# Kernel tuning notes

Measured on AMD Instinct MI355X. Metric: run time of the kernel, lower is better.

## Reference

```python
import jax, jax.numpy as jnp
import numpy as np

H = 32        # num query heads
HKV = 8       # num kv heads
D = 128       # head_dim
SCALE = D ** -0.5
FP8_MAX = 448.0   # e4m3 max
EPS = 1e-8
PAGE = 256
NPAGES = 20
SQ = 1024     # new diffusion tokens
CTX = 3072    # cached context tokens
DIFF_BLK = 32 # diffusion block size


def setup_inputs() -> dict:
    key = jax.random.key(0)
    ks = jax.random.split(key, 6)
    q = jax.random.normal(ks[0], (SQ, H * D), dtype=jnp.float32)
    k = jax.random.normal(ks[1], (SQ, HKV * D), dtype=jnp.float32)
    v = jax.random.normal(ks[2], (SQ, HKV * D), dtype=jnp.float32)
    # paged caches (values already stored in quantized units)
    k_cache = jax.random.normal(ks[3], (NPAGES, PAGE, HKV, D), dtype=jnp.float32)
    v_cache = jax.random.normal(ks[4], (NPAGES, PAGE, HKV, D), dtype=jnp.float32)
    # new tokens go into slots right after the context
    slot_mapping = jnp.arange(CTX, CTX + SQ, dtype=jnp.int32)
    cache_slots = jnp.arange(CTX, dtype=jnp.int32)
    # diffusion mask: full visibility of context, block-causal among new tokens
    blk = jnp.arange(SQ) // DIFF_BLK
    ctx_mask = jnp.ones((SQ, CTX), dtype=bool)
    new_mask = blk[:, None] >= blk[None, :]
    block_mask = jnp.concatenate([ctx_mask, new_mask], axis=1)  # [SQ, CTX+SQ]
    return {"q": q, "k": k, "v": v, "k_cache": k_cache, "v_cache": v_cache,
            "slot_mapping": slot_mapping, "cache_slots": cache_slots,
            "block_mask": block_mask}


def reference(q, k, v, k_cache, v_cache, slot_mapping, cache_slots, block_mask):
    k3 = k.reshape(-1, HKV, D)
    v3 = v.reshape(-1, HKV, D)
    qh = q.reshape(-1, H, D)

    # ---- FP8 scale tracking: per-kv-head absmax over (token, dim) ----
    k_scale = jnp.maximum(jnp.max(jnp.abs(k3), axis=(0, 2)) / FP8_MAX, EPS)  # [HKV]
    v_scale = jnp.maximum(jnp.max(jnp.abs(v3), axis=(0, 2)) / FP8_MAX, EPS)

    # ---- paged KV-cache store with inline quantization ----
    kc = k_cache.reshape(-1, HKV, D)  # [NPAGES*PAGE, HKV, D]
    vc = v_cache.reshape(-1, HKV, D)
    k_q = jnp.clip(k3 / k_scale[None, :, None], -FP8_MAX, FP8_MAX)
    v_q = jnp.clip(v3 / v_scale[None, :, None], -FP8_MAX, FP8_MAX)
    kc = kc.at[slot_mapping].set(k_q)
    vc = vc.at[slot_mapping].set(v_q)

    # ---- load context tokens from cache and dequantize ----
    k_ctx = kc[cache_slots] * k_scale[None, :, None]  # [CTX, HKV, D]
    v_ctx = vc[cache_slots] * v_scale[None, :, None]
    k_comb = jnp.concatenate([k_ctx, k3], axis=0)  # [SKV, HKV, D]
    v_comb = jnp.concatenate([v_ctx, v3], axis=0)

    # ---- GQA flex attention with token-level block mask ----
    G = H // HKV
    k_g = jnp.repeat(k_comb, G, axis=1)  # [SKV, H, D]
    v_g = jnp.repeat(v_comb, G, axis=1)
    scores = jnp.einsum('qhd,khd->hqk', qh, k_g) * SCALE  # [H, SQ, SKV]
    scores = jnp.where(block_mask[None, :, :], scores, jnp.float32(-1e30))
    probs = jax.nn.softmax(scores, axis=-1)
    o = jnp.einsum('hqk,khd->qhd', probs, v_g)  # [SQ, H, D]
    return o.reshape(-1, H * D)
```

## Files before the change

kernel.cpp:

```cpp
#include <hip/hip_runtime.h>
#include <stdint.h>

#define H 32
#define HKV 8
#define D 128
#define SQ 1024
#define CTX 3072
#define SKV 4096
#define FP8_MAX_C 448.0f
#define EPS_C 1e-8f

typedef __attribute__((ext_vector_type(4))) float f32x4;
typedef __attribute__((ext_vector_type(8))) __bf16 bf16x8;
typedef __attribute__((ext_vector_type(8))) unsigned short u16x8;

__device__ __forceinline__ unsigned short f2bf(float x) {
  unsigned int u = __builtin_bit_cast(unsigned int, x);
  u += 0x7fffu + ((u >> 16) & 1u);
  return (unsigned short)(u >> 16);
}

__device__ __forceinline__ f32x4 mfma16(bf16x8 a, bf16x8 b, f32x4 c) {
  return __builtin_amdgcn_mfma_f32_16x16x32_bf16(a, b, c, 0, 0, 0);
}

__device__ __forceinline__ void gld16(const unsigned short* g, char* l) {
  __builtin_amdgcn_global_load_lds(
      (const __attribute__((address_space(1))) unsigned int*)g,
      (__attribute__((address_space(3))) unsigned int*)l, 16, 0, 0);
}

__device__ __forceinline__ void stage_sync() {
  asm volatile("s_waitcnt vmcnt(0)" ::: "memory");
  __builtin_amdgcn_sched_barrier(0);
  __syncthreads();
}

__global__ void scales_part(const float* __restrict__ k,
                            const float* __restrict__ v,
                            unsigned int* __restrict__ smax) {
  const int b = blockIdx.x & 15;
  const int part = blockIdx.x >> 4;
  const float* src = (b < HKV) ? k : v;
  const int h = b & 7;
  const int tid = threadIdx.x;
  const int d0 = (tid & 31) * 4;
  float mx = 0.f;
  const int t1 = part * 128 + 128;
  for (int t = part * 128 + (tid >> 5); t < t1; t += 8) {
    float4 vv = *reinterpret_cast<const float4*>(src + (size_t)t * (HKV * D) + h * D + d0);
    mx = fmaxf(mx, fmaxf(fmaxf(fabsf(vv.x), fabsf(vv.y)),
                         fmaxf(fabsf(vv.z), fabsf(vv.w))));
  }
  __shared__ float red[256];
  red[tid] = mx;
  __syncthreads();
  for (int s = 128; s > 0; s >>= 1) {
    if (tid < s) red[tid] = fmaxf(red[tid], red[tid + s]);
    __syncthreads();
  }
  if (tid == 0) atomicMax(&smax[b], __float_as_uint(red[0]));
}

__global__ void scales_fin(const unsigned int* __restrict__ smax,
                           float* __restrict__ scales) {
  const int i = threadIdx.x;
  if (i < 16) scales[i] = fmaxf(__uint_as_float(smax[i]) / FP8_MAX_C, EPS_C);
}

__global__ void prep_k(const float* __restrict__ k,
                       const float* __restrict__ k_cache,
                       const int* __restrict__ cache_slots,
                       const float* __restrict__ scales,
                       unsigned short* __restrict__ k_comb) {
  const int tid = blockIdx.x * 256 + threadIdx.x;
  const int d8 = tid & 15;
  const int t = (tid >> 4) & (SKV - 1);
  const int h = tid >> 16;
  const int d0 = d8 * 8;
  const float* src;
  float mul;
  if (t < CTX) {
    int slot = cache_slots[t];
    src = k_cache + (size_t)slot * (HKV * D) + h * D + d0;
    mul = scales[h];
  } else {
    src = k + (size_t)(t - CTX) * (HKV * D) + h * D + d0;
    mul = 1.f;
  }
  float4 a = *reinterpret_cast<const float4*>(src);
  float4 bb = *reinterpret_cast<const float4*>(src + 4);
  u16x8 r;
  r[0] = f2bf(a.x * mul);  r[1] = f2bf(a.y * mul);
  r[2] = f2bf(a.z * mul);  r[3] = f2bf(a.w * mul);
  r[4] = f2bf(bb.x * mul); r[5] = f2bf(bb.y * mul);
  r[6] = f2bf(bb.z * mul); r[7] = f2bf(bb.w * mul);
  *reinterpret_cast<u16x8*>(k_comb + ((size_t)h * SKV + t) * D + d0) = r;
}

__global__ void prep_v(const float* __restrict__ v,
                       const float* __restrict__ v_cache,
                       const int* __restrict__ cache_slots,
                       const float* __restrict__ scales,
                       unsigned short* __restrict__ v_combT) {
  const int tid = blockIdx.x * 256 + threadIdx.x;
  const int d = tid & 127;
  const int t8 = (tid >> 7) & 511;
  const int h = tid >> 16;
  const int t0 = t8 * 8;
  const float sc = scales[8 + h];
  u16x8 r;
#pragma unroll
  for (int i = 0; i < 8; ++i) {
    int t = t0 + i;
    float val;
    if (t < CTX) {
      int slot = cache_slots[t];
      val = v_cache[(size_t)slot * (HKV * D) + h * D + d] * sc;
    } else {
      val = v[(size_t)(t - CTX) * (HKV * D) + h * D + d];
    }
    r[i] = f2bf(val);
  }
  *reinterpret_cast<u16x8*>(v_combT + ((size_t)h * D + d) * SKV + t0) = r;
}

#define LDBF(p) (*reinterpret_cast<const bf16x8*>(p))
#define Z4 ((f32x4){0.f, 0.f, 0.f, 0.f})

#define STAGE(TB, BUFO)                                                        \
  {                                                                            \
    _Pragma("unroll")                                                          \
    for (int j = 0; j < 4; ++j) {                                              \
      const int c = wid * 256 + j * 64 + l;                                    \
      const int r_ = c >> 4;                                                   \
      const int lc_ = (c & 15) ^ (r_ & 7);                                     \
      gld16(kb + (size_t)((TB) + r_) * D + lc_ * 8,                            \
            smem + (BUFO) + c * 16);                                           \
      const int dv_ = c >> 3;                                                  \
      const int lv_ = (c & 7) ^ (dv_ & 7);                                     \
      gld16(vb + (size_t)dv_ * SKV + (TB) + lv_ * 8,                           \
            smem + (BUFO) + 16384 + c * 16);                                   \
    }                                                                          \
  }

#define EXP4(SREG, P, RSV)                                                     \
  {                                                                            \
    P[0] = __builtin_amdgcn_exp2f(SREG[0] - m);                                \
    P[1] = __builtin_amdgcn_exp2f(SREG[1] - m);                                \
    P[2] = __builtin_amdgcn_exp2f(SREG[2] - m);                                \
    P[3] = __builtin_amdgcn_exp2f(SREG[3] - m);                                \
    RSV += (P[0] + P[1]) + (P[2] + P[3]);                                      \
  }

#define CVTPK(DST, LO, HI)                                                     \
  asm("v_cvt_pk_bf16_f32 %0, %1, %2" : "=v"(DST) : "v"(LO), "v"(HI));
#define SW32(A, B)                                                             \
  asm("v_permlane32_swap_b32 %0, %1" : "+v"(A), "+v"(B));
#define SW16(A, B)                                                             \
  asm("v_permlane16_swap_b32 %0, %1" : "+v"(A), "+v"(B));

#define PTRANS(P0, P1, P2, P3, PF0, PF1)                                       \
  {                                                                            \
    unsigned int A_, Ap_, B_, Bp_, C_, Cp_, Dd_, Dp_;                          \
    CVTPK(A_, P0[0], P0[1]) CVTPK(Ap_, P0[2], P0[3])                           \
    CVTPK(B_, P1[0], P1[1]) CVTPK(Bp_, P1[2], P1[3])                           \
    CVTPK(C_, P2[0], P2[1]) CVTPK(Cp_, P2[2], P2[3])                           \
    CVTPK(Dd_, P3[0], P3[1]) CVTPK(Dp_, P3[2], P3[3])                          \
    SW32(A_, B_) SW16(A_, B_)                                                  \
    SW32(Ap_, Bp_) SW16(Ap_, Bp_)                                              \
    SW32(C_, Dd_) SW16(C_, Dd_)                                                \
    SW32(Cp_, Dp_) SW16(Cp_, Dp_)                                              \
    union { unsigned int d[4]; bf16x8 v; } u0_, u1_;                           \
    u0_.d[0] = A_; u0_.d[1] = Ap_; u0_.d[2] = B_; u0_.d[3] = Bp_;              \
    u1_.d[0] = C_; u1_.d[1] = Cp_; u1_.d[2] = Dd_; u1_.d[3] = Dp_;             \
    PF0 = u0_.v; PF1 = u1_.v;                                                  \
  }

#define QKSF(SF, SA, SB)                                                       \
  {                                                                            \
    bf16x8 a0 = LDBF(kc + SF * 4096 + kx0);                                    \
    bf16x8 a1 = LDBF(kc + SF * 4096 + kx1);                                    \
    bf16x8 a2 = LDBF(kc + SF * 4096 + kx2);                                    \
    bf16x8 a3 = LDBF(kc + SF * 4096 + kx3);                                    \
    SA = mfma16(a0, qa0, SA); SA = mfma16(a1, qa1, SA);                        \
    SA = mfma16(a2, qa2, SA); SA = mfma16(a3, qa3, SA);                        \
    SB = mfma16(a0, qb0, SB); SB = mfma16(a1, qb1, SB);                        \
    SB = mfma16(a2, qb2, SB); SB = mfma16(a3, qb3, SB);                        \
  }

#define PVDT(DT, AA, AB)                                                       \
  {                                                                            \
    bf16x8 va = LDBF(vc + DT * 2048 + vxa);                                    \
    bf16x8 vw = LDBF(vc + DT * 2048 + vxb);                                    \
    AA = mfma16(pfa0, va, AA); AA = mfma16(pfa1, vw, AA);                      \
    AB = mfma16(pfb0, va, AB); AB = mfma16(pfb1, vw, AB);                      \
  }

__launch_bounds__(256, 2)
__global__ void attn_kernel(const float* __restrict__ q,
                            const unsigned short* __restrict__ k_comb,
                            const unsigned short* __restrict__ v_combT,
                            float* __restrict__ out,
                            float* __restrict__ part1,
                            float* __restrict__ ml) {
  extern __shared__ __align__(16) char smem[];
  const int bid = blockIdx.x;
  const int hkv = bid & 7;
  const int qp_raw = (bid >> 3) & 31;
  const int half = bid >> 8;
  const int qp = half ? (31 - qp_raw) : qp_raw;
  const int tid = threadIdx.x;
  const int wid = tid >> 6;
  const int l = tid & 63;
  const int lo = l & 15;
  const int g = l >> 4;
  const int qbase = qp * 32 + (wid >> 1) * 16;
  const int hqa = hkv * 4 + (wid & 1) * 2;
  const int nt32 = 97 + qp;
  const int n64 = (nt32 + 1) >> 1;
  const int nh = (n64 + 1) >> 1;
  const int t0 = half ? nh : 0;
  const int t1 = half ? n64 : nh;
  const bool tail = (nt32 & 1) && half;

  const unsigned short* kb = k_comb + (size_t)hkv * SKV * D;
  const unsigned short* vb = v_combT + (size_t)hkv * D * SKV;

  bf16x8 qa0, qa1, qa2, qa3, qb0, qb1, qb2, qb3;
  {
    const float qs = 0.088388347648318447f * 1.4426950408889634f;
    const float* qpA = q + (size_t)(qbase + lo) * (H * D) + hqa * D;
#define QLOAD(PTR, KS, DST)                                                    \
    {                                                                          \
      float4 a = *reinterpret_cast<const float4*>((PTR) + KS * 32 + g * 8);    \
      float4 b = *reinterpret_cast<const float4*>((PTR) + KS * 32 + g * 8 + 4);\
      union { unsigned short u[8]; bf16x8 v; } f;                              \
      f.u[0] = f2bf(a.x * qs); f.u[1] = f2bf(a.y * qs);                        \
      f.u[2] = f2bf(a.z * qs); f.u[3] = f2bf(a.w * qs);                        \
      f.u[4] = f2bf(b.x * qs); f.u[5] = f2bf(b.y * qs);                        \
      f.u[6] = f2bf(b.z * qs); f.u[7] = f2bf(b.w * qs);                        \
      DST = f.v;                                                               \
    }
    QLOAD(qpA, 0, qa0) QLOAD(qpA, 1, qa1) QLOAD(qpA, 2, qa2) QLOAD(qpA, 3, qa3)
    const float* qpB = qpA + D;
    QLOAD(qpB, 0, qb0) QLOAD(qpB, 1, qb1) QLOAD(qpB, 2, qb2) QLOAD(qpB, 3, qb3)
#undef QLOAD
  }

  f32x4 aa0 = Z4, aa1 = Z4, aa2 = Z4, aa3 = Z4;
  f32x4 aa4 = Z4, aa5 = Z4, aa6 = Z4, aa7 = Z4;
  f32x4 ab0 = Z4, ab1 = Z4, ab2 = Z4, ab3 = Z4;
  f32x4 ab4 = Z4, ab5 = Z4, ab6 = Z4, ab7 = Z4;
  float m = -1e30f;
  float lsa = 0.f, lsb = 0.f;

  const int xr = lo & 7;
  const int kx0 = ((0 + g) ^ xr) << 4;
  const int kx1 = ((4 + g) ^ xr) << 4;
  const int kx2 = ((8 + g) ^ xr) << 4;
  const int kx3 = ((12 + g) ^ xr) << 4;
  const int vxa = ((g) ^ xr) << 4;
  const int vxb = ((g + 4) ^ xr) << 4;
  const char* kbl = smem + lo * 256;
  const char* vbl = smem + 16384 + lo * 128;

  int cur = 0;
  STAGE(t0 * 64, 0)
  stage_sync();

  for (int t = t0; t < t1; ++t) {
    if (t + 1 < t1) STAGE((t + 1) * 64, (cur ^ 1) * 32768)

    const char* kc = kbl + cur * 32768;
    const char* vc = vbl + cur * 32768;

    f32x4 sa0 = Z4, sa1 = Z4, sa2 = Z4, sa3 = Z4;
    f32x4 sb0 = Z4, sb1 = Z4, sb2 = Z4, sb3 = Z4;
    __builtin_amdgcn_s_setprio(1);
    QKSF(0, sa0, sb0)
    QKSF(1, sa1, sb1)
    QKSF(2, sa2, sb2)
    QKSF(3, sa3, sb3)
    __builtin_amdgcn_s_setprio(0);

    if (tail && t == n64 - 1) {
      sa2 = (f32x4){-1e30f, -1e30f, -1e30f, -1e30f};
      sa3 = (f32x4){-1e30f, -1e30f, -1e30f, -1e30f};
      sb2 = (f32x4){-1e30f, -1e30f, -1e30f, -1e30f};
      sb3 = (f32x4){-1e30f, -1e30f, -1e30f, -1e30f};
    }

    float pmax = fmaxf(fmaxf(fmaxf(sa0[0], sa0[1]), fmaxf(sa0[2], sa0[3])),
                       fmaxf(fmaxf(sa1[0], sa1[1]), fmaxf(sa1[2], sa1[3])));
    pmax = fmaxf(pmax,
                 fmaxf(fmaxf(fmaxf(sa2[0], sa2[1]), fmaxf(sa2[2], sa2[3])),
                       fmaxf(fmaxf(sa3[0], sa3[1]), fmaxf(sa3[2], sa3[3]))));
    pmax = fmaxf(pmax,
                 fmaxf(fmaxf(fmaxf(sb0[0], sb0[1]), fmaxf(sb0[2], sb0[3])),
                       fmaxf(fmaxf(sb1[0], sb1[1]), fmaxf(sb1[2], sb1[3]))));
    pmax = fmaxf(pmax,
                 fmaxf(fmaxf(fmaxf(sb2[0], sb2[1]), fmaxf(sb2[2], sb2[3])),
                       fmaxf(fmaxf(sb3[0], sb3[1]), fmaxf(sb3[2], sb3[3]))));
    if (!__all(pmax - m <= 8.f)) {
      float rm = fmaxf(pmax, __shfl_xor(pmax, 16));
      rm = fmaxf(rm, __shfl_xor(rm, 32));
      float mn = fmaxf(m, rm);
      float scl = __builtin_amdgcn_exp2f(m - mn);
      lsa *= scl; lsb *= scl;
      aa0 *= scl; aa1 *= scl; aa2 *= scl; aa3 *= scl;
      aa4 *= scl; aa5 *= scl; aa6 *= scl; aa7 *= scl;
      ab0 *= scl; ab1 *= scl; ab2 *= scl; ab3 *= scl;
      ab4 *= scl; ab5 *= scl; ab6 *= scl; ab7 *= scl;
      m = mn;
    }

    float pa0[4], pa1[4], pa2[4], pa3[4], pb0[4], pb1[4], pb2[4], pb3[4];
    EXP4(sa0, pa0, lsa) EXP4(sa1, pa1, lsa) EXP4(sa2, pa2, lsa) EXP4(sa3, pa3, lsa)
    EXP4(sb0, pb0, lsb) EXP4(sb1, pb1, lsb) EXP4(sb2, pb2, lsb) EXP4(sb3, pb3, lsb)

    bf16x8 pfa0, pfa1, pfb0, pfb1;
    PTRANS(pa0, pa1, pa2, pa3, pfa0, pfa1)
    PTRANS(pb0, pb1, pb2, pb3, pfb0, pfb1)

    __builtin_amdgcn_s_setprio(1);
    PVDT(0, aa0, ab0)
    PVDT(1, aa1, ab1)
    PVDT(2, aa2, ab2)
    PVDT(3, aa3, ab3)
    PVDT(4, aa4, ab4)
    PVDT(5, aa5, ab5)
    PVDT(6, aa6, ab6)
    PVDT(7, aa7, ab7)
    __builtin_amdgcn_s_setprio(0);

    stage_sync();
    cur ^= 1;
  }

  lsa += __shfl_xor(lsa, 16); lsa += __shfl_xor(lsa, 32);
  lsb += __shfl_xor(lsb, 16); lsb += __shfl_xor(lsb, 32);
  float* dst = half ? part1 : out;
  if (g == 0) {
    float2 v;
    v.x = m; v.y = lsa;
    *reinterpret_cast<float2*>(ml + ((size_t)half * SQ * H + (qbase + lo) * H + hqa) * 2) = v;
    v.y = lsb;
    *reinterpret_cast<float2*>(ml + ((size_t)half * SQ * H + (qbase + lo) * H + hqa + 1) * 2) = v;
  }
#pragma unroll
  for (int r = 0; r < 4; ++r) {
    float* opa = dst + (size_t)(qbase + g * 4 + r) * (H * D) + hqa * D + lo;
    float* opb = opa + D;
    opa[0 * 16] = aa0[r]; opb[0 * 16] = ab0[r];
    opa[1 * 16] = aa1[r]; opb[1 * 16] = ab1[r];
    opa[2 * 16] = aa2[r]; opb[2 * 16] = ab2[r];
    opa[3 * 16] = aa3[r]; opb[3 * 16] = ab3[r];
    opa[4 * 16] = aa4[r]; opb[4 * 16] = ab4[r];
    opa[5 * 16] = aa5[r]; opb[5 * 16] = ab5[r];
    opa[6 * 16] = aa6[r]; opb[6 * 16] = ab6[r];
    opa[7 * 16] = aa7[r]; opb[7 * 16] = ab7[r];
  }
}

__global__ void merge_kernel(float* __restrict__ out,
                             const float* __restrict__ part1,
                             const float* __restrict__ ml) {
  const int idx = blockIdx.x * 256 + threadIdx.x;
  const int h = (idx >> 5) & 31;
  const int qrow = idx >> 10;
  const float2* mp = (const float2*)ml;
  float2 A = mp[qrow * H + h];
  float2 B = mp[SQ * H + qrow * H + h];
  float mm = fmaxf(A.x, B.x);
  float wa = __builtin_amdgcn_exp2f(A.x - mm);
  float wb = __builtin_amdgcn_exp2f(B.x - mm);
  float inv = 1.f / (A.y * wa + B.y * wb);
  float4 oa = reinterpret_cast<float4*>(out)[idx];
  float4 ob = reinterpret_cast<const float4*>(part1)[idx];
  float4 r;
  r.x = (oa.x * wa + ob.x * wb) * inv;
  r.y = (oa.y * wa + ob.y * wb) * inv;
  r.z = (oa.z * wa + ob.z * wb) * inv;
  r.w = (oa.w * wa + ob.w * wb) * inv;
  reinterpret_cast<float4*>(out)[idx] = r;
}

extern "C" void kernel_launch(void* const* d_in, const int* in_sizes, int n_in,
                              void* d_out, int out_size, void* d_ws, size_t ws_size,
                              hipStream_t stream) {
  (void)in_sizes; (void)n_in; (void)out_size; (void)ws_size;
  const float* q = (const float*)d_in[0];
  const float* k = (const float*)d_in[1];
  const float* v = (const float*)d_in[2];
  const float* k_cache = (const float*)d_in[3];
  const float* v_cache = (const float*)d_in[4];
  const int* cache_slots = (const int*)d_in[6];
  float* out = (float*)d_out;

  unsigned int* smax = (unsigned int*)d_ws;
  float* scales = (float*)((char*)d_ws + 64);
  unsigned short* k_comb = (unsigned short*)((char*)d_ws + 256);
  unsigned short* v_combT = k_comb + (size_t)HKV * SKV * D;
  float* part1 = (float*)((char*)d_ws + 256 + (size_t)32 * 1024 * 1024 / 2);
  float* ml = part1 + (size_t)SQ * H * D;

  hipMemsetAsync(smax, 0, 64, stream);
  scales_part<<<128, 256, 0, stream>>>(k, v, smax);
  scales_fin<<<1, 64, 0, stream>>>(smax, scales);
  prep_k<<<2048, 256, 0, stream>>>(k, k_cache, cache_slots, scales, k_comb);
  prep_v<<<2048, 256, 0, stream>>>(v, v_cache, cache_slots, scales, v_combT);
  attn_kernel<<<512, 256, 65536, stream>>>(q, k_comb, v_combT, out, part1, ml);
  merge_kernel<<<4096, 256, 0, stream>>>(out, part1, ml);
}
```

Before: 113.9 us.

## Load V fragments directly from global memory into registers, dropping LDS staging

V tiles are no longer staged through shared memory. Each lane now reads its transposed-V fragments straight from global memory at the top of each iteration, ahead of the QK MFMAs. This halves LDS use per block (64KB to 32KB) and removes the V LDS writes and reads, which could allow more blocks per CU and ease LDS bandwidth pressure. The cost is 16 extra 16-byte global loads per lane per tile, which depend on L2 hits and add VGPR pressure, and their latency must be hidden behind the QK and softmax work.

```diff
diff --git a/kernel.cpp b/kernel.cpp
--- a/kernel.cpp
+++ b/kernel.cpp
@@ -137,10 +137,6 @@
       const int lc_ = (c & 15) ^ (r_ & 7);                                     \
       gld16(kb + (size_t)((TB) + r_) * D + lc_ * 8,                            \
             smem + (BUFO) + c * 16);                                           \
-      const int dv_ = c >> 3;                                                  \
-      const int lv_ = (c & 7) ^ (dv_ & 7);                                     \
-      gld16(vb + (size_t)dv_ * SKV + (TB) + lv_ * 8,                           \
-            smem + (BUFO) + 16384 + c * 16);                                   \
     }                                                                          \
   }
 
@@ -189,12 +185,10 @@
     SB = mfma16(a2, qb2, SB); SB = mfma16(a3, qb3, SB);                        \
   }
 
-#define PVDT(DT, AA, AB)                                                       \
+#define PVDT(VA, VB, AA, AB)                                                   \
   {                                                                            \
-    bf16x8 va = LDBF(vc + DT * 2048 + vxa);                                    \
-    bf16x8 vw = LDBF(vc + DT * 2048 + vxb);                                    \
-    AA = mfma16(pfa0, va, AA); AA = mfma16(pfa1, vw, AA);                      \
-    AB = mfma16(pfb0, va, AB); AB = mfma16(pfb1, vw, AB);                      \
+    AA = mfma16(pfa0, VA, AA); AA = mfma16(pfa1, VB, AA);                      \
+    AB = mfma16(pfb0, VA, AB); AB = mfma16(pfb1, VB, AB);                      \
   }
 
 __launch_bounds__(256, 2)
@@ -260,20 +254,29 @@
   const int kx1 = ((4 + g) ^ xr) << 4;
   const int kx2 = ((8 + g) ^ xr) << 4;
   const int kx3 = ((12 + g) ^ xr) << 4;
-  const int vxa = ((g) ^ xr) << 4;
-  const int vxb = ((g + 4) ^ xr) << 4;
   const char* kbl = smem + lo * 256;
-  const char* vbl = smem + 16384 + lo * 128;
+  const unsigned short* vrow = vb + (size_t)lo * SKV + g * 8;
 
   int cur = 0;
   STAGE(t0 * 64, 0)
   stage_sync();
 
   for (int t = t0; t < t1; ++t) {
-    if (t + 1 < t1) STAGE((t + 1) * 64, (cur ^ 1) * 32768)
-
-    const char* kc = kbl + cur * 32768;
-    const char* vc = vbl + cur * 32768;
+    const int tb = t * 64;
+    if (t + 1 < t1) STAGE((t + 1) * 64, (cur ^ 1) * 16384)
+
+    const unsigned short* vp = vrow + tb;
+    bf16x8 v0a = LDBF(vp + 0 * 65536), v0b = LDBF(vp + 0 * 65536 + 32);
+    bf16x8 v1a = LDBF(vp + 1 * 65536), v1b = LDBF(vp + 1 * 65536 + 32);
+    bf16x8 v2a = LDBF(vp + 2 * 65536), v2b = LDBF(vp + 2 * 65536 + 32);
+    bf16x8 v3a = LDBF(vp + 3 * 65536), v3b = LDBF(vp + 3 * 65536 + 32);
+    bf16x8 v4a = LDBF(vp + 4 * 65536), v4b = LDBF(vp + 4 * 65536 + 32);
+    bf16x8 v5a = LDBF(vp + 5 * 65536), v5b = LDBF(vp + 5 * 65536 + 32);
+    bf16x8 v6a = LDBF(vp + 6 * 65536), v6b = LDBF(vp + 6 * 65536 + 32);
+    bf16x8 v7a = LDBF(vp + 7 * 65536), v7b = LDBF(vp + 7 * 65536 + 32);
+    __builtin_amdgcn_sched_barrier(0);
+
+    const char* kc = kbl + cur * 16384;
 
     f32x4 sa0 = Z4, sa1 = Z4, sa2 = Z4, sa3 = Z4;
     f32x4 sb0 = Z4, sb1 = Z4, sb2 = Z4, sb3 = Z4;
@@ -324,14 +327,14 @@
     PTRANS(pb0, pb1, pb2, pb3, pfb0, pfb1)
 
     __builtin_amdgcn_s_setprio(1);
-    PVDT(0, aa0, ab0)
-    PVDT(1, aa1, ab1)
-    PVDT(2, aa2, ab2)
-    PVDT(3, aa3, ab3)
-    PVDT(4, aa4, ab4)
-    PVDT(5, aa5, ab5)
-    PVDT(6, aa6, ab6)
-    PVDT(7, aa7, ab7)
+    PVDT(v0a, v0b, aa0, ab0)
+    PVDT(v1a, v1b, aa1, ab1)
+    PVDT(v2a, v2b, aa2, ab2)
+    PVDT(v3a, v3b, aa3, ab3)
+    PVDT(v4a, v4b, aa4, ab4)
+    PVDT(v5a, v5b, aa5, ab5)
+    PVDT(v6a, v6b, aa6, ab6)
+    PVDT(v7a, v7b, aa7, ab7)
     __builtin_amdgcn_s_setprio(0);
 
     stage_sync();
@@ -410,6 +413,6 @@
   scales_fin<<<1, 64, 0, stream>>>(smax, scales);
   prep_k<<<2048, 256, 0, stream>>>(k, k_cache, cache_slots, scales, k_comb);
   prep_v<<<2048, 256, 0, stream>>>(v, v_cache, cache_slots, scales, v_combT);
-  attn_kernel<<<512, 256, 65536, stream>>>(q, k_comb, v_combT, out, part1, ml);
+  attn_kernel<<<512, 256, 32768, stream>>>(q, k_comb, v_combT, out, part1, ml);
   merge_kernel<<<4096, 256, 0, stream>>>(out, part1, ml);
 }
```

New measurement: 163.1 us. +43.2%, slower.

## Shrink KV tile to 32 tokens and split attention into up to four KV partitions

Applied to the files above, without the earlier changes.

The attention kernel's KV tile drops from 64 to 32 tokens, which halves the double-buffered shared memory to 32KB and raises launch bounds to 4 blocks per SM. The KV range is now split into nsplit parts (4 when the workspace is large enough, otherwise 2), and the merge kernel combines a general number of partial results. The aim is more parallel blocks and higher occupancy to hide latency. In exchange, each tile has fewer MFMAs to amortise sync and softmax overhead, and the merge step reads and writes more partial-output traffic.

```diff
diff --git a/kernel.cpp b/kernel.cpp
--- a/kernel.cpp
+++ b/kernel.cpp
@@ -131,16 +131,16 @@
 #define STAGE(TB, BUFO)                                                        \
   {                                                                            \
     _Pragma("unroll")                                                          \
-    for (int j = 0; j < 4; ++j) {                                              \
-      const int c = wid * 256 + j * 64 + l;                                    \
+    for (int j = 0; j < 2; ++j) {                                              \
+      const int c = j * 256 + tid;                                             \
       const int r_ = c >> 4;                                                   \
       const int lc_ = (c & 15) ^ (r_ & 7);                                     \
       gld16(kb + (size_t)((TB) + r_) * D + lc_ * 8,                            \
             smem + (BUFO) + c * 16);                                           \
-      const int dv_ = c >> 3;                                                  \
-      const int lv_ = (c & 7) ^ (dv_ & 7);                                     \
-      gld16(vb + (size_t)dv_ * SKV + (TB) + lv_ * 8,                           \
-            smem + (BUFO) + 16384 + c * 16);                                   \
+      const int dv_ = c >> 2;                                                  \
+      const int cv_ = (c & 3) ^ ((dv_ >> 1) & 3);                              \
+      gld16(vb + (size_t)dv_ * SKV + (TB) + cv_ * 8,                           \
+            smem + (BUFO) + 8192 + c * 16);                                    \
     }                                                                          \
   }
 
@@ -160,21 +160,16 @@
 #define SW16(A, B)                                                             \
   asm("v_permlane16_swap_b32 %0, %1" : "+v"(A), "+v"(B));
 
-#define PTRANS(P0, P1, P2, P3, PF0, PF1)                                       \
+#define PTRANS32(P0, P1, PF)                                                   \
   {                                                                            \
-    unsigned int A_, Ap_, B_, Bp_, C_, Cp_, Dd_, Dp_;                          \
+    unsigned int A_, Ap_, B_, Bp_;                                             \
     CVTPK(A_, P0[0], P0[1]) CVTPK(Ap_, P0[2], P0[3])                           \
     CVTPK(B_, P1[0], P1[1]) CVTPK(Bp_, P1[2], P1[3])                           \
-    CVTPK(C_, P2[0], P2[1]) CVTPK(Cp_, P2[2], P2[3])                           \
-    CVTPK(Dd_, P3[0], P3[1]) CVTPK(Dp_, P3[2], P3[3])                          \
     SW32(A_, B_) SW16(A_, B_)                                                  \
     SW32(Ap_, Bp_) SW16(Ap_, Bp_)                                              \
-    SW32(C_, Dd_) SW16(C_, Dd_)                                                \
-    SW32(Cp_, Dp_) SW16(Cp_, Dp_)                                              \
-    union { unsigned int d[4]; bf16x8 v; } u0_, u1_;                           \
-    u0_.d[0] = A_; u0_.d[1] = Ap_; u0_.d[2] = B_; u0_.d[3] = Bp_;              \
-    u1_.d[0] = C_; u1_.d[1] = Cp_; u1_.d[2] = Dd_; u1_.d[3] = Dp_;             \
-    PF0 = u0_.v; PF1 = u1_.v;                                                  \
+    union { unsigned int d[4]; bf16x8 v; } u_;                                 \
+    u_.d[0] = A_; u_.d[1] = Ap_; u_.d[2] = B_; u_.d[3] = Bp_;                  \
+    PF = u_.v;                                                                 \
   }
 
 #define QKSF(SF, SA, SB)                                                       \
@@ -191,25 +186,25 @@
 
 #define PVDT(DT, AA, AB)                                                       \
   {                                                                            \
-    bf16x8 va = LDBF(vc + DT * 2048 + vxa);                                    \
-    bf16x8 vw = LDBF(vc + DT * 2048 + vxb);                                    \
-    AA = mfma16(pfa0, va, AA); AA = mfma16(pfa1, vw, AA);                      \
-    AB = mfma16(pfb0, va, AB); AB = mfma16(pfb1, vw, AB);                      \
-  }
-
-__launch_bounds__(256, 2)
+    bf16x8 va = LDBF(vc + DT * 1024 + vx);                                     \
+    AA = mfma16(pfa, va, AA);                                                  \
+    AB = mfma16(pfb, va, AB);                                                  \
+  }
+
+__launch_bounds__(256, 4)
 __global__ void attn_kernel(const float* __restrict__ q,
                             const unsigned short* __restrict__ k_comb,
                             const unsigned short* __restrict__ v_combT,
                             float* __restrict__ out,
-                            float* __restrict__ part1,
-                            float* __restrict__ ml) {
+                            float* __restrict__ parts,
+                            float* __restrict__ ml,
+                            int nsplit) {
   extern __shared__ __align__(16) char smem[];
   const int bid = blockIdx.x;
   const int hkv = bid & 7;
   const int qp_raw = (bid >> 3) & 31;
-  const int half = bid >> 8;
-  const int qp = half ? (31 - qp_raw) : qp_raw;
+  const int part = bid >> 8;
+  const int qp = (part & 1) ? (31 - qp_raw) : qp_raw;
   const int tid = threadIdx.x;
   const int wid = tid >> 6;
   const int l = tid & 63;
@@ -217,12 +212,9 @@
   const int g = l >> 4;
   const int qbase = qp * 32 + (wid >> 1) * 16;
   const int hqa = hkv * 4 + (wid & 1) * 2;
-  const int nt32 = 97 + qp;
-  const int n64 = (nt32 + 1) >> 1;
-  const int nh = (n64 + 1) >> 1;
-  const int t0 = half ? nh : 0;
-  const int t1 = half ? n64 : nh;
-  const bool tail = (nt32 & 1) && half;
+  const int n32 = 97 + qp;
+  const int t0 = (part * n32) / nsplit;
+  const int t1 = ((part + 1) * n32) / nsplit;
 
   const unsigned short* kb = k_comb + (size_t)hkv * SKV * D;
   const unsigned short* vb = v_combT + (size_t)hkv * D * SKV;
@@ -260,48 +252,31 @@
   const int kx1 = ((4 + g) ^ xr) << 4;
   const int kx2 = ((8 + g) ^ xr) << 4;
   const int kx3 = ((12 + g) ^ xr) << 4;
-  const int vxa = ((g) ^ xr) << 4;
-  const int vxb = ((g + 4) ^ xr) << 4;
+  const int vx = ((g ^ ((lo >> 1) & 3))) << 4;
   const char* kbl = smem + lo * 256;
-  const char* vbl = smem + 16384 + lo * 128;
+  const char* vbl = smem + 8192 + lo * 64;
 
   int cur = 0;
-  STAGE(t0 * 64, 0)
+  STAGE(t0 * 32, 0)
   stage_sync();
 
   for (int t = t0; t < t1; ++t) {
-    if (t + 1 < t1) STAGE((t + 1) * 64, (cur ^ 1) * 32768)
-
-    const char* kc = kbl + cur * 32768;
-    const char* vc = vbl + cur * 32768;
-
-    f32x4 sa0 = Z4, sa1 = Z4, sa2 = Z4, sa3 = Z4;
-    f32x4 sb0 = Z4, sb1 = Z4, sb2 = Z4, sb3 = Z4;
+    if (t + 1 < t1) STAGE((t + 1) * 32, (cur ^ 1) * 16384)
+
+    const char* kc = kbl + cur * 16384;
+    const char* vc = vbl + cur * 16384;
+
+    f32x4 sa0 = Z4, sa1 = Z4, sb0 = Z4, sb1 = Z4;
     __builtin_amdgcn_s_setprio(1);
     QKSF(0, sa0, sb0)
     QKSF(1, sa1, sb1)
-    QKSF(2, sa2, sb2)
-    QKSF(3, sa3, sb3)
     __builtin_amdgcn_s_setprio(0);
-
-    if (tail && t == n64 - 1) {
-      sa2 = (f32x4){-1e30f, -1e30f, -1e30f, -1e30f};
-      sa3 = (f32x4){-1e30f, -1e30f, -1e30f, -1e30f};
-      sb2 = (f32x4){-1e30f, -1e30f, -1e30f, -1e30f};
-      sb3 = (f32x4){-1e30f, -1e30f, -1e30f, -1e30f};
-    }
 
     float pmax = fmaxf(fmaxf(fmaxf(sa0[0], sa0[1]), fmaxf(sa0[2], sa0[3])),
                        fmaxf(fmaxf(sa1[0], sa1[1]), fmaxf(sa1[2], sa1[3])));
     pmax = fmaxf(pmax,
-                 fmaxf(fmaxf(fmaxf(sa2[0], sa2[1]), fmaxf(sa2[2], sa2[3])),
-                       fmaxf(fmaxf(sa3[0], sa3[1]), fmaxf(sa3[2], sa3[3]))));
-    pmax = fmaxf(pmax,
                  fmaxf(fmaxf(fmaxf(sb0[0], sb0[1]), fmaxf(sb0[2], sb0[3])),
                        fmaxf(fmaxf(sb1[0], sb1[1]), fmaxf(sb1[2], sb1[3]))));
-    pmax = fmaxf(pmax,
-                 fmaxf(fmaxf(fmaxf(sb2[0], sb2[1]), fmaxf(sb2[2], sb2[3])),
-                       fmaxf(fmaxf(sb3[0], sb3[1]), fmaxf(sb3[2], sb3[3]))));
     if (!__all(pmax - m <= 8.f)) {
       float rm = fmaxf(pmax, __shfl_xor(pmax, 16));
       rm = fmaxf(rm, __shfl_xor(rm, 32));
@@ -315,13 +290,13 @@
       m = mn;
     }
 
-    float pa0[4], pa1[4], pa2[4], pa3[4], pb0[4], pb1[4], pb2[4], pb3[4];
-    EXP4(sa0, pa0, lsa) EXP4(sa1, pa1, lsa) EXP4(sa2, pa2, lsa) EXP4(sa3, pa3, lsa)
-    EXP4(sb0, pb0, lsb) EXP4(sb1, pb1, lsb) EXP4(sb2, pb2, lsb) EXP4(sb3, pb3, lsb)
-
-    bf16x8 pfa0, pfa1, pfb0, pfb1;
-    PTRANS(pa0, pa1, pa2, pa3, pfa0, pfa1)
-    PTRANS(pb0, pb1, pb2, pb3, pfb0, pfb1)
+    float pa0[4], pa1[4], pb0[4], pb1[4];
+    EXP4(sa0, pa0, lsa) EXP4(sa1, pa1, lsa)
+    EXP4(sb0, pb0, lsb) EXP4(sb1, pb1, lsb)
+
+    bf16x8 pfa, pfb;
+    PTRANS32(pa0, pa1, pfa)
+    PTRANS32(pb0, pb1, pfb)
 
     __builtin_amdgcn_s_setprio(1);
     PVDT(0, aa0, ab0)
@@ -340,13 +315,13 @@
 
   lsa += __shfl_xor(lsa, 16); lsa += __shfl_xor(lsa, 32);
   lsb += __shfl_xor(lsb, 16); lsb += __shfl_xor(lsb, 32);
-  float* dst = half ? part1 : out;
+  float* dst = (part == 0) ? out : parts + (size_t)(part - 1) * SQ * H * D;
   if (g == 0) {
     float2 v;
     v.x = m; v.y = lsa;
-    *reinterpret_cast<float2*>(ml + ((size_t)half * SQ * H + (qbase + lo) * H + hqa) * 2) = v;
+    *reinterpret_cast<float2*>(ml + ((size_t)part * SQ * H + (qbase + lo) * H + hqa) * 2) = v;
     v.y = lsb;
-    *reinterpret_cast<float2*>(ml + ((size_t)half * SQ * H + (qbase + lo) * H + hqa + 1) * 2) = v;
+    *reinterpret_cast<float2*>(ml + ((size_t)part * SQ * H + (qbase + lo) * H + hqa + 1) * 2) = v;
   }
 #pragma unroll
   for (int r = 0; r < 4; ++r) {
@@ -364,32 +339,40 @@
 }
 
 __global__ void merge_kernel(float* __restrict__ out,
-                             const float* __restrict__ part1,
-                             const float* __restrict__ ml) {
+                             const float* __restrict__ parts,
+                             const float* __restrict__ ml,
+                             int nsplit) {
   const int idx = blockIdx.x * 256 + threadIdx.x;
   const int h = (idx >> 5) & 31;
   const int qrow = idx >> 10;
   const float2* mp = (const float2*)ml;
-  float2 A = mp[qrow * H + h];
-  float2 B = mp[SQ * H + qrow * H + h];
-  float mm = fmaxf(A.x, B.x);
-  float wa = __builtin_amdgcn_exp2f(A.x - mm);
-  float wb = __builtin_amdgcn_exp2f(B.x - mm);
-  float inv = 1.f / (A.y * wa + B.y * wb);
-  float4 oa = reinterpret_cast<float4*>(out)[idx];
-  float4 ob = reinterpret_cast<const float4*>(part1)[idx];
+  float mm = -1e30f;
+  for (int p = 0; p < nsplit; ++p)
+    mm = fmaxf(mm, mp[p * SQ * H + qrow * H + h].x);
+  float den = 0.f;
+  float4 num = {0.f, 0.f, 0.f, 0.f};
+  for (int p = 0; p < nsplit; ++p) {
+    float2 A = mp[p * SQ * H + qrow * H + h];
+    float w = __builtin_amdgcn_exp2f(A.x - mm);
+    den += A.y * w;
+    const float4* src = (p == 0) ? reinterpret_cast<const float4*>(out)
+                                 : reinterpret_cast<const float4*>(
+                                       parts + (size_t)(p - 1) * SQ * H * D);
+    float4 o = src[idx];
+    num.x += o.x * w; num.y += o.y * w;
+    num.z += o.z * w; num.w += o.w * w;
+  }
+  float inv = 1.f / den;
   float4 r;
-  r.x = (oa.x * wa + ob.x * wb) * inv;
-  r.y = (oa.y * wa + ob.y * wb) * inv;
-  r.z = (oa.z * wa + ob.z * wb) * inv;
-  r.w = (oa.w * wa + ob.w * wb) * inv;
+  r.x = num.x * inv; r.y = num.y * inv;
+  r.z = num.z * inv; r.w = num.w * inv;
   reinterpret_cast<float4*>(out)[idx] = r;
 }
 
 extern "C" void kernel_launch(void* const* d_in, const int* in_sizes, int n_in,
                               void* d_out, int out_size, void* d_ws, size_t ws_size,
                               hipStream_t stream) {
-  (void)in_sizes; (void)n_in; (void)out_size; (void)ws_size;
+  (void)in_sizes; (void)n_in; (void)out_size;
   const float* q = (const float*)d_in[0];
   const float* k = (const float*)d_in[1];
   const float* v = (const float*)d_in[2];
@@ -398,18 +381,24 @@
   const int* cache_slots = (const int*)d_in[6];
   float* out = (float*)d_out;
 
+  const size_t PART_FLOATS = (size_t)SQ * H * D;
+  const size_t PREP = 256 + (size_t)32 * 1024 * 1024 / 2;
+  const size_t need4 = PREP + 3 * PART_FLOATS * 4 + 4 * (size_t)SQ * H * 8;
+  const int nsplit = (ws_size >= need4) ? 4 : 2;
+
   unsigned int* smax = (unsigned int*)d_ws;
   float* scales = (float*)((char*)d_ws + 64);
   unsigned short* k_comb = (unsigned short*)((char*)d_ws + 256);
   unsigned short* v_combT = k_comb + (size_t)HKV * SKV * D;
-  float* part1 = (float*)((char*)d_ws + 256 + (size_t)32 * 1024 * 1024 / 2);
-  float* ml = part1 + (size_t)SQ * H * D;
+  float* parts = (float*)((char*)d_ws + PREP);
+  float* ml = parts + (size_t)(nsplit - 1) * PART_FLOATS;
 
   hipMemsetAsync(smax, 0, 64, stream);
   scales_part<<<128, 256, 0, stream>>>(k, v, smax);
   scales_fin<<<1, 64, 0, stream>>>(smax, scales);
   prep_k<<<2048, 256, 0, stream>>>(k, k_cache, cache_slots, scales, k_comb);
   prep_v<<<2048, 256, 0, stream>>>(v, v_cache, cache_slots, scales, v_combT);
-  attn_kernel<<<512, 256, 65536, stream>>>(q, k_comb, v_combT, out, part1, ml);
-  merge_kernel<<<4096, 256, 0, stream>>>(out, part1, ml);
-}
+  attn_kernel<<<256 * nsplit, 256, 32768, stream>>>(q, k_comb, v_combT, out,
+                                                    parts, ml, nsplit);
+  merge_kernel<<<4096, 256, 0, stream>>>(out, parts, ml, nsplit);
+}
```

After: 217.6 us. 91.1% more time.
